# Kernel tuning notes

Hardware: AMD Instinct MI355X
Metric: run time of the kernel (lower is better)

Reference implementation:

```python
import jax, jax.numpy as jnp
import numpy as np


def _analytic_phase(x):
    """FFT-based analytic-signal phase, mean over channels. x: (B, C, T) -> (B, T)."""
    B, C, T = x.shape
    Xf = jnp.fft.fft(x, axis=-1)  # complex64
    # Hilbert multiplier: h[0]=1, h[1:T//2]=2, h[T//2]=1 (T even), rest 0
    h = np.zeros((T,), dtype=np.float32)
    h[0] = 1.0
    h[1:T // 2] = 2.0
    if T % 2 == 0:
        h[T // 2] = 1.0
    analytic = jnp.fft.ifft(Xf * jnp.asarray(h), axis=-1)
    phase = jnp.angle(analytic)          # (B, C, T)
    return phase.mean(axis=1)            # (B, T)


def setup_inputs() -> dict:
    key = jax.random.key(0)
    k = jax.random.split(key, 6)
    B, C, T = 32, 9, 4096
    num_codes, code_dim = 512, 64
    half = code_dim // 2
    s = 1.0 / np.sqrt(C)  # kaiming-uniform-ish scale for Linear(9, .)
    return {
        "imu_signal": jax.random.normal(k[0], (B, C, T), dtype=jnp.float32),
        "W_mag": jax.random.uniform(k[1], (half, C), jnp.float32, -s, s),
        "b_mag": jax.random.uniform(k[2], (half,), jnp.float32, -s, s),
        "W_phase": jax.random.uniform(k[3], (half, C), jnp.float32, -s, s),
        "b_phase": jax.random.uniform(k[4], (half,), jnp.float32, -s, s),
        "codebook": jax.random.normal(k[5], (num_codes, code_dim), dtype=jnp.float32),
    }


def reference(imu_signal, W_mag, b_mag, W_phase, b_phase, codebook):
    # imu_signal: (B, 9, T)
    phases = _analytic_phase(imu_signal)                      # (B, T)
    imu_btc = jnp.transpose(imu_signal, (0, 2, 1))            # (B, T, 9)

    mag_features = imu_btc @ W_mag.T + b_mag                  # (B, T, 32)

    phase_input = jnp.stack([jnp.cos(phases), jnp.sin(phases)], axis=-1)  # (B, T, 2)
    combined = jnp.concatenate([imu_btc[:, :, :7], phase_input], axis=-1)  # (B, T, 9)
    phase_features = combined @ W_phase.T + b_phase           # (B, T, 32)

    features = jnp.concatenate([mag_features, phase_features], axis=-1)  # (B, T, 64)

    # cdist argmin == argmin of squared distances: ||f||^2 - 2 f.c + ||c||^2
    d2 = (jnp.sum(features * features, axis=-1, keepdims=True)
          - 2.0 * jnp.einsum("btd,kd->btk", features, codebook)
          + jnp.sum(codebook * codebook, axis=-1))            # (B, T, K)
    indices = jnp.argmin(d2, axis=-1)                         # (B, T)
    quantized = codebook[indices]                             # (B, T, 64)
    return quantized, indices, phases
```

## Files before the change

### kernel.cpp

```cpp
#include <hip/hip_runtime.h>
#include <math.h>

#define TN 4096
#define HN 2048
#define NB 32
#define NCH 9
#define NCODES 512
#define CDIM 64
#define TAU 1e-3f
#define PTS 256
#define VQT 512

typedef _Float16 f16x8 __attribute__((ext_vector_type(8)));
typedef float f32x4 __attribute__((ext_vector_type(4)));

__device__ __forceinline__ float2 cmulf(float2 a, float2 b) {
    return make_float2(a.x * b.x - a.y * b.y, a.x * b.y + a.y * b.x);
}
__device__ __forceinline__ float2 f2add(float2 a, float2 b) {
    return make_float2(a.x + b.x, a.y + b.y);
}
__device__ __forceinline__ float2 f2sub(float2 a, float2 b) {
    return make_float2(a.x - b.x, a.y - b.y);
}

__device__ __forceinline__ unsigned long long packsi(float s, int i) {
    unsigned u = __float_as_uint(s);
    u = (u & 0x80000000u) ? ~u : (u | 0x80000000u);
    return ((unsigned long long)u << 32) | (unsigned)i;
}

__device__ __forceinline__ size_t aunit(int pbase, int plane, int s, int hi16, int l15) {
    return ((size_t)(((pbase * 2 + plane) * 2 + s) * 4 + hi16) << 4) + l15;
}

__global__ __launch_bounds__(256) void prep_kernel(const float* __restrict__ cb,
                                                   float* __restrict__ cn,
                                                   f16x8* __restrict__ ctiles,
                                                   float* __restrict__ ph) {
    const int bid = blockIdx.x;
    const int tid = threadIdx.x;
    if (bid < 512) {
        ph[bid * 256 + tid] = 0.0f;
        return;
    }
    if (bid < 544) {
        const int u = (bid - 512) * 256 + tid;
        const int l15 = u & 15;
        const int hi16 = (u >> 4) & 3;
        const int s = (u >> 6) & 1;
        const int plane = (u >> 7) & 1;
        const int cbase = u >> 8;
        const int code = cbase * 16 + l15;
        f16x8 out;
        #pragma unroll
        for (int e = 0; e < 8; ++e) {
            float c = cb[code * CDIM + 32 * s + 8 * hi16 + e];
            _Float16 hh = (_Float16)c;
            out[e] = plane ? (_Float16)(c - (float)hh) : hh;
        }
        ctiles[u] = out;
        return;
    }
    for (int k = tid; k < NCODES; k += 256) {
        const float4* c4 = (const float4*)(cb + (size_t)k * CDIM);
        float s = 0.0f;
        #pragma unroll
        for (int q = 0; q < 16; ++q) {
            float4 c = c4[q];
            s = fmaf(c.x, c.x, s);
            s = fmaf(c.y, c.y, s);
            s = fmaf(c.z, c.z, s);
            s = fmaf(c.w, c.w, s);
        }
        cn[k] = s;
    }
}

#define HT 512
__global__ __launch_bounds__(HT) void hilbert_phase_kernel(
    const float* __restrict__ x, float* __restrict__ phases) {
    __shared__ float2 bufA[TN];
    __shared__ float2 bufB[TN];
    __shared__ float2 tw[HN];
    const int tid = threadIdx.x;
    const int row1 = 2 * blockIdx.x;
    const int row2 = row1 + 1;
    const int b1 = row1 / NCH;
    const int b2 = row2 / NCH;
    const float* xr1 = x + (size_t)row1 * TN;
    const float* xr2 = x + (size_t)row2 * TN;

    for (int i = tid; i < HN; i += HT) {
        float ang = -3.14159265358979323846f * ((float)i / (float)HN);
        float s, c;
        sincosf(ang, &s, &c);
        tw[i] = make_float2(c, s);
    }
    for (int i = tid; i < TN; i += HT) {
        bufA[i] = make_float2(xr1[i], xr2[i]);
    }
    __syncthreads();

    float2* src = bufA;
    float2* dst = bufB;
    for (int stage = 0; stage < 6; ++stage) {
        const int m = 1 << (2 * stage);
        for (int idx = tid; idx < 1024; idx += HT) {
            const int kk = idx & (m - 1);
            const int jm = idx - kk;
            float2 a0 = src[idx];
            float2 a1 = src[idx + 1024];
            float2 a2 = src[idx + 2048];
            float2 a3 = src[idx + 3072];
            float2 b0 = f2add(a0, a2);
            float2 b1 = f2add(a1, a3);
            float2 b2 = f2sub(a0, a2);
            float2 b3 = f2sub(a1, a3);
            float2 w1 = tw[jm];
            float2 w2 = tw[2 * jm];
            float2 w3 = cmulf(w1, w2);
            float2 y0 = f2add(b0, b1);
            float2 mi = make_float2(b2.x + b3.y, b2.y - b3.x);
            float2 pi_ = make_float2(b2.x - b3.y, b2.y + b3.x);
            dst[4 * jm + kk]         = y0;
            dst[4 * jm + kk + m]     = cmulf(mi, w1);
            dst[4 * jm + kk + 2 * m] = cmulf(f2sub(b0, b1), w2);
            dst[4 * jm + kk + 3 * m] = cmulf(pi_, w3);
        }
        __syncthreads();
        float2* t0 = src; src = dst; dst = t0;
    }
    const float inv = 1.0f / (float)TN;
    for (int i = tid; i < TN; i += HT) {
        float sc;
        if (i == 0 || i == HN) sc = inv;
        else if (i < HN) sc = 2.0f * inv;
        else sc = 0.0f;
        float2 v = src[i];
        v.x *= sc; v.y *= sc;
        src[i] = v;
    }
    __syncthreads();
    for (int stage = 0; stage < 6; ++stage) {
        const int m = 1 << (2 * stage);
        for (int idx = tid; idx < 1024; idx += HT) {
            const int kk = idx & (m - 1);
            const int jm = idx - kk;
            float2 a0 = src[idx];
            float2 a1 = src[idx + 1024];
            float2 a2 = src[idx + 2048];
            float2 a3 = src[idx + 3072];
            float2 b0 = f2add(a0, a2);
            float2 b1 = f2add(a1, a3);
            float2 b2 = f2sub(a0, a2);
            float2 b3 = f2sub(a1, a3);
            float2 w1 = tw[jm];      w1.y = -w1.y;
            float2 w2 = tw[2 * jm];  w2.y = -w2.y;
            float2 w3 = cmulf(w1, w2);
            float2 y0 = f2add(b0, b1);
            float2 pi_ = make_float2(b2.x - b3.y, b2.y + b3.x);
            float2 mi = make_float2(b2.x + b3.y, b2.y - b3.x);
            dst[4 * jm + kk]         = y0;
            dst[4 * jm + kk + m]     = cmulf(pi_, w1);
            dst[4 * jm + kk + 2 * m] = cmulf(f2sub(b0, b1), w2);
            dst[4 * jm + kk + 3 * m] = cmulf(mi, w3);
        }
        __syncthreads();
        float2* t0 = src; src = dst; dst = t0;
    }
    float* ph1 = phases + (size_t)b1 * TN;
    float* ph2 = phases + (size_t)b2 * TN;
    for (int i = tid; i < TN; i += HT) {
        float2 d = src[i];
        float x1v = xr1[i];
        float x2v = xr2[i];
        atomicAdd(&ph1[i], atan2f(d.y - x2v, x1v) * (1.0f / 9.0f));
        atomicAdd(&ph2[i], atan2f(x1v - d.x, x2v) * (1.0f / 9.0f));
    }
}

__global__ __launch_bounds__(256) void feat_kernel(
    const float* __restrict__ imu,
    const float* __restrict__ Wm, const float* __restrict__ bm,
    const float* __restrict__ Wp, const float* __restrict__ bp,
    const float* __restrict__ phases,
    f16x8* __restrict__ atiles) {
    const int p = blockIdx.x * 256 + threadIdx.x;
    const int bb = p >> 12;
    const int tt = p & (TN - 1);
    float xc[9];
    #pragma unroll
    for (int c = 0; c < 9; ++c)
        xc[c] = imu[((size_t)(bb * 9 + c)) * TN + tt];
    float sp, cp;
    sincosf(phases[p], &sp, &cp);

    const int pbase = p >> 4;
    const int l15 = p & 15;
    #pragma unroll
    for (int g = 0; g < 8; ++g) {
        float v8[8];
        if (g < 4) {
            #pragma unroll
            for (int e = 0; e < 8; ++e) {
                const int j = 8 * g + e;
                float a = bm[j];
                #pragma unroll
                for (int c = 0; c < 9; ++c) a = fmaf(Wm[j * 9 + c], xc[c], a);
                v8[e] = a;
            }
        } else {
            #pragma unroll
            for (int e = 0; e < 8; ++e) {
                const int j = 8 * (g - 4) + e;
                float a = bp[j];
                #pragma unroll
                for (int c = 0; c < 7; ++c) a = fmaf(Wp[j * 9 + c], xc[c], a);
                a = fmaf(Wp[j * 9 + 7], cp, a);
                a = fmaf(Wp[j * 9 + 8], sp, a);
                v8[e] = a;
            }
        }
        f16x8 hv, lv;
        #pragma unroll
        for (int e = 0; e < 8; ++e) {
            _Float16 hh = (_Float16)v8[e];
            hv[e] = hh;
            lv[e] = (_Float16)(v8[e] - (float)hh);
        }
        const int s = g >> 2;
        const int hi16 = g & 3;
        atiles[aunit(pbase, 0, s, hi16, l15)] = hv;
        atiles[aunit(pbase, 1, s, hi16, l15)] = lv;
    }
}

#define MFMA16(A, B, C) __builtin_amdgcn_mfma_f32_16x16x32_f16((A), (B), (C), 0, 0, 0)

__global__ __launch_bounds__(VQT, 4) void vq_kernel(
    const float* __restrict__ imu,
    const float* __restrict__ Wm, const float* __restrict__ bm,
    const float* __restrict__ Wp, const float* __restrict__ bp,
    const float* __restrict__ cb,
    const float* __restrict__ cn,
    const f16x8* __restrict__ ctiles,
    const float* __restrict__ phases,
    const f16x8* atiles,
    float* out_q,
    float* __restrict__ out_i) {
    __shared__ float s_b[16][PTS];
    __shared__ float s_s[16][PTS];
    __shared__ int   s_i[16][PTS];
    __shared__ int s_idx[PTS];
    __shared__ float s_gap[PTS];
    const int tid = threadIdx.x;
    const int lane = tid & 63;
    const int w = tid >> 6;
    const int l15 = lane & 15;
    const int hi16 = lane >> 4;
    const int p0 = blockIdx.x * PTS;
    const int pb0 = p0 >> 4;

    for (int h = 0; h < 2; ++h) {
        const int kbase = 64 * w + 32 * h;
        const int cb0 = kbase >> 4;
        f16x8 cH00 = ctiles[aunit(cb0 + 0, 0, 0, hi16, l15)];
        f16x8 cH01 = ctiles[aunit(cb0 + 0, 0, 1, hi16, l15)];
        f16x8 cH10 = ctiles[aunit(cb0 + 1, 0, 0, hi16, l15)];
        f16x8 cH11 = ctiles[aunit(cb0 + 1, 0, 1, hi16, l15)];
        f16x8 cL00 = ctiles[aunit(cb0 + 0, 1, 0, hi16, l15)];
        f16x8 cL01 = ctiles[aunit(cb0 + 0, 1, 1, hi16, l15)];
        f16x8 cL10 = ctiles[aunit(cb0 + 1, 1, 0, hi16, l15)];
        f16x8 cL11 = ctiles[aunit(cb0 + 1, 1, 1, hi16, l15)];
        f32x4 cnv0 = *(const f32x4*)(cn + kbase + 4 * hi16);
        f32x4 cnv1 = *(const f32x4*)(cn + kbase + 16 + 4 * hi16);
        asm volatile("" : "+v"(cH00), "+v"(cH01), "+v"(cH10), "+v"(cH11),
                          "+v"(cL00), "+v"(cL01), "+v"(cL10), "+v"(cL11));
        asm volatile("" : "+v"(cnv0), "+v"(cnv1));

        #pragma unroll 2
        for (int cf = 0; cf < 16; ++cf) {
            const int pbase = pb0 + cf;
            f16x8 bH0 = atiles[aunit(pbase, 0, 0, hi16, l15)];
            f16x8 bH1 = atiles[aunit(pbase, 0, 1, hi16, l15)];
            f16x8 bL0 = atiles[aunit(pbase, 1, 0, hi16, l15)];
            f16x8 bL1 = atiles[aunit(pbase, 1, 1, hi16, l15)];
            f32x4 a0 = (f32x4){0.f, 0.f, 0.f, 0.f};
            f32x4 a1 = (f32x4){0.f, 0.f, 0.f, 0.f};
            a0 = MFMA16(cH00, bH0, a0);
            a0 = MFMA16(cH00, bL0, a0);
            a0 = MFMA16(cL00, bH0, a0);
            a0 = MFMA16(cH01, bH1, a0);
            a0 = MFMA16(cH01, bL1, a0);
            a0 = MFMA16(cL01, bH1, a0);
            a1 = MFMA16(cH10, bH0, a1);
            a1 = MFMA16(cH10, bL0, a1);
            a1 = MFMA16(cL10, bH0, a1);
            a1 = MFMA16(cH11, bH1, a1);
            a1 = MFMA16(cH11, bL1, a1);
            a1 = MFMA16(cL11, bH1, a1);
            float b = 3.4e38f, sec = 3.4e38f;
            int bi = 0;
            #pragma unroll
            for (int r = 0; r < 4; ++r) {
                float sc = fmaf(-2.0f, a0[r], cnv0[r]);
                const int ci = kbase + 4 * hi16 + r;
                bool lt = sc < b;
                sec = fminf(sec, lt ? b : sc);
                b = lt ? sc : b;
                bi = lt ? ci : bi;
            }
            #pragma unroll
            for (int r = 0; r < 4; ++r) {
                float sc = fmaf(-2.0f, a1[r], cnv1[r]);
                const int ci = kbase + 16 + 4 * hi16 + r;
                bool lt = sc < b;
                sec = fminf(sec, lt ? b : sc);
                b = lt ? sc : b;
                bi = lt ? ci : bi;
            }
            #pragma unroll
            for (int m = 16; m <= 32; m <<= 1) {
                float ob = __shfl_xor(b, m, 64);
                float os = __shfl_xor(sec, m, 64);
                int oi = __shfl_xor(bi, m, 64);
                float mx = fmaxf(b, ob);
                sec = fminf(fminf(sec, os), mx);
                bool take = (ob < b) || (ob == b && oi < bi);
                b = take ? ob : b;
                bi = take ? oi : bi;
            }
            if (hi16 == 0) {
                s_b[2 * w + h][16 * cf + l15] = b;
                s_s[2 * w + h][16 * cf + l15] = sec;
                s_i[2 * w + h][16 * cf + l15] = bi;
            }
        }
    }
    __syncthreads();

    if (tid < PTS) {
        float b = 3.4e38f, sec = 3.4e38f;
        int bi = 0;
        #pragma unroll 4
        for (int q = 0; q < 16; ++q) {
            float ob = s_b[q][tid];
            float os = s_s[q][tid];
            int oi = s_i[q][tid];
            float mx = fmaxf(b, ob);
            sec = fminf(fminf(sec, os), mx);
            bool take = (ob < b) || (ob == b && oi < bi);
            b = take ? ob : b;
            bi = take ? oi : bi;
        }
        s_idx[tid] = bi;
        out_i[p0 + tid] = (float)bi;
        s_gap[tid] = sec - b;
    }
    __syncthreads();

    {
        bool fl = (lane < 32) && (s_gap[32 * w + (lane & 31)] < TAU);
        unsigned long long bal = __ballot(fl);
        while (bal) {
            const int ln = __builtin_ctzll(bal);
            bal &= bal - 1;
            const int row = 32 * w + ln;
            const int pR = p0 + row;
            const int bbR = pR >> 12;
            const int ttR = pR & (TN - 1);
            float xcR[9];
            #pragma unroll
            for (int c = 0; c < 9; ++c)
                xcR[c] = imu[((size_t)(bbR * 9 + c)) * TN + ttR];
            float spR, cpR;
            sincosf(phases[pR], &spR, &cpR);
            float a0[8], a1[8], a2[8], a3[8];
            #pragma unroll
            for (int cc = 0; cc < 8; ++cc) {
                a0[cc] = 0.f; a1[cc] = 0.f; a2[cc] = 0.f; a3[cc] = 0.f;
            }
            for (int d4 = 0; d4 < 16; ++d4) {
                float fd[4];
                #pragma unroll
                for (int e = 0; e < 4; ++e) {
                    const int j = 4 * d4 + e;
                    float a;
                    if (j < 32) {
                        a = bm[j];
                        #pragma unroll
                        for (int c = 0; c < 9; ++c) a = fmaf(Wm[j * 9 + c], xcR[c], a);
                    } else {
                        const int jj = j - 32;
                        a = bp[jj];
                        #pragma unroll
                        for (int c = 0; c < 7; ++c) a = fmaf(Wp[jj * 9 + c], xcR[c], a);
                        a = fmaf(Wp[jj * 9 + 7], cpR, a);
                        a = fmaf(Wp[jj * 9 + 8], spR, a);
                    }
                    fd[e] = a;
                }
                #pragma unroll
                for (int cc = 0; cc < 8; ++cc) {
                    const float4 cv = ((const float4*)(cb + (size_t)(lane * 8 + cc) * CDIM))[d4];
                    a0[cc] = fmaf(fd[0], cv.x, a0[cc]);
                    a1[cc] = fmaf(fd[1], cv.y, a1[cc]);
                    a2[cc] = fmaf(fd[2], cv.z, a2[cc]);
                    a3[cc] = fmaf(fd[3], cv.w, a3[cc]);
                }
            }
            unsigned long long pbest = ~0ull;
            #pragma unroll
            for (int cc = 0; cc < 8; ++cc) {
                const int kk = lane * 8 + cc;
                float sc = fmaf(-2.0f, (a0[cc] + a1[cc]) + (a2[cc] + a3[cc]), cn[kk]);
                unsigned long long pk = packsi(sc, kk);
                pbest = pk < pbest ? pk : pbest;
            }
            #pragma unroll
            for (int m = 1; m <= 32; m <<= 1) {
                unsigned long long o = __shfl_xor(pbest, m, 64);
                pbest = o < pbest ? o : pbest;
            }
            if (lane == 0) {
                const int bi = (int)(pbest & 0xFFFFFFFFu);
                s_idx[row] = bi;
                out_i[p0 + row] = (float)bi;
            }
        }
    }
    __syncthreads();

    float4* oq = (float4*)out_q;
    const float4* c4g = (const float4*)cb;
    for (int i = tid; i < PTS * 16; i += VQT) {
        const int pt = i >> 4;
        const int q = i & 15;
        oq[(size_t)(p0 + pt) * 16 + q] = c4g[(size_t)s_idx[pt] * 16 + q];
    }
}

extern "C" void kernel_launch(void* const* d_in, const int* in_sizes, int n_in,
                              void* d_out, int out_size, void* d_ws, size_t ws_size,
                              hipStream_t stream) {
    const float* imu = (const float*)d_in[0];
    const float* Wm  = (const float*)d_in[1];
    const float* bm  = (const float*)d_in[2];
    const float* Wp  = (const float*)d_in[3];
    const float* bp  = (const float*)d_in[4];
    const float* cb  = (const float*)d_in[5];

    float* out_q = (float*)d_out;
    float* out_i = out_q + (size_t)NB * TN * CDIM;
    float* out_p = out_i + (size_t)NB * TN;

    float* cn     = (float*)d_ws;
    f16x8* ctiles = (f16x8*)((char*)d_ws + 2048);
    f16x8* atiles = (f16x8*)out_q;

    prep_kernel<<<545, 256, 0, stream>>>(cb, cn, ctiles, out_p);
    hilbert_phase_kernel<<<NB * NCH / 2, HT, 0, stream>>>(imu, out_p);
    feat_kernel<<<(NB * TN) / 256, 256, 0, stream>>>(imu, Wm, bm, Wp, bp, out_p, atiles);
    vq_kernel<<<(NB * TN) / PTS, VQT, 0, stream>>>(imu, Wm, bm, Wp, bp, cb,
                                                   cn, ctiles, out_p, atiles,
                                                   out_q, out_i);
}
```

Measured before the change: 171.9 us.

## Stage point tiles in LDS and widen per-wave code tile to 64 codes

The VQ kernel now copies the block's 256-point split-f16 feature tiles into shared memory with async global-to-LDS loads, instead of each wave re-reading them from global memory twice. Each wave keeps 64 codes' hi/lo fragments in registers and computes four 16x16 accumulators per point group in one pass. This halves the partial-argmin slots to merge. More resident registers and 64KB of LDS drop the occupancy hint from 4 to 2 blocks per CU, trading occupancy for less redundant memory traffic.

```diff
diff --git a/kernel.cpp b/kernel.cpp
--- a/kernel.cpp
+++ b/kernel.cpp
@@ -28,6 +28,12 @@
     unsigned u = __float_as_uint(s);
     u = (u & 0x80000000u) ? ~u : (u | 0x80000000u);
     return ((unsigned long long)u << 32) | (unsigned)i;
+}
+
+__device__ __forceinline__ void gload_lds16(const void* g, void* l) {
+    __builtin_amdgcn_global_load_lds(
+        (const __attribute__((address_space(1))) unsigned int*)g,
+        (__attribute__((address_space(3))) unsigned int*)l, 16, 0, 0);
 }
 
 __device__ __forceinline__ size_t aunit(int pbase, int plane, int s, int hi16, int l15) {
@@ -238,7 +244,7 @@
 
 #define MFMA16(A, B, C) __builtin_amdgcn_mfma_f32_16x16x32_f16((A), (B), (C), 0, 0, 0)
 
-__global__ __launch_bounds__(VQT, 4) void vq_kernel(
+__global__ __launch_bounds__(VQT, 2) void vq_kernel(
     const float* __restrict__ imu,
     const float* __restrict__ Wm, const float* __restrict__ bm,
     const float* __restrict__ Wp, const float* __restrict__ bp,
@@ -249,9 +255,10 @@
     const f16x8* atiles,
     float* out_q,
     float* __restrict__ out_i) {
-    __shared__ float s_b[16][PTS];
-    __shared__ float s_s[16][PTS];
-    __shared__ int   s_i[16][PTS];
+    __shared__ __align__(16) f16x8 sPT[16 * 256];
+    __shared__ float s_b[8][PTS];
+    __shared__ float s_s[8][PTS];
+    __shared__ int   s_i[8][PTS];
     __shared__ int s_idx[PTS];
     __shared__ float s_gap[PTS];
     const int tid = threadIdx.x;
@@ -262,80 +269,78 @@
     const int p0 = blockIdx.x * PTS;
     const int pb0 = p0 >> 4;
 
-    for (int h = 0; h < 2; ++h) {
-        const int kbase = 64 * w + 32 * h;
-        const int cb0 = kbase >> 4;
-        f16x8 cH00 = ctiles[aunit(cb0 + 0, 0, 0, hi16, l15)];
-        f16x8 cH01 = ctiles[aunit(cb0 + 0, 0, 1, hi16, l15)];
-        f16x8 cH10 = ctiles[aunit(cb0 + 1, 0, 0, hi16, l15)];
-        f16x8 cH11 = ctiles[aunit(cb0 + 1, 0, 1, hi16, l15)];
-        f16x8 cL00 = ctiles[aunit(cb0 + 0, 1, 0, hi16, l15)];
-        f16x8 cL01 = ctiles[aunit(cb0 + 0, 1, 1, hi16, l15)];
-        f16x8 cL10 = ctiles[aunit(cb0 + 1, 1, 0, hi16, l15)];
-        f16x8 cL11 = ctiles[aunit(cb0 + 1, 1, 1, hi16, l15)];
-        f32x4 cnv0 = *(const f32x4*)(cn + kbase + 4 * hi16);
-        f32x4 cnv1 = *(const f32x4*)(cn + kbase + 16 + 4 * hi16);
-        asm volatile("" : "+v"(cH00), "+v"(cH01), "+v"(cH10), "+v"(cH11),
-                          "+v"(cL00), "+v"(cL01), "+v"(cL10), "+v"(cL11));
-        asm volatile("" : "+v"(cnv0), "+v"(cnv1));
-
-        #pragma unroll 2
-        for (int cf = 0; cf < 16; ++cf) {
-            const int pbase = pb0 + cf;
-            f16x8 bH0 = atiles[aunit(pbase, 0, 0, hi16, l15)];
-            f16x8 bH1 = atiles[aunit(pbase, 0, 1, hi16, l15)];
-            f16x8 bL0 = atiles[aunit(pbase, 1, 0, hi16, l15)];
-            f16x8 bL1 = atiles[aunit(pbase, 1, 1, hi16, l15)];
-            f32x4 a0 = (f32x4){0.f, 0.f, 0.f, 0.f};
-            f32x4 a1 = (f32x4){0.f, 0.f, 0.f, 0.f};
-            a0 = MFMA16(cH00, bH0, a0);
-            a0 = MFMA16(cH00, bL0, a0);
-            a0 = MFMA16(cL00, bH0, a0);
-            a0 = MFMA16(cH01, bH1, a0);
-            a0 = MFMA16(cH01, bL1, a0);
-            a0 = MFMA16(cL01, bH1, a0);
-            a1 = MFMA16(cH10, bH0, a1);
-            a1 = MFMA16(cH10, bL0, a1);
-            a1 = MFMA16(cL10, bH0, a1);
-            a1 = MFMA16(cH11, bH1, a1);
-            a1 = MFMA16(cH11, bL1, a1);
-            a1 = MFMA16(cL11, bH1, a1);
-            float b = 3.4e38f, sec = 3.4e38f;
-            int bi = 0;
+    {
+        const char* gsrc = (const char*)(atiles + (size_t)pb0 * 256);
+        char* ldst = (char*)sPT;
+        #pragma unroll
+        for (int i = 0; i < 8; ++i) {
+            const int u = i * VQT + tid;
+            gload_lds16(gsrc + (size_t)u * 16, ldst + u * 16);
+        }
+    }
+
+    const int kbase = 64 * w;
+    f16x8 cH[4][2], cL[4][2];
+    #pragma unroll
+    for (int rf = 0; rf < 4; ++rf) {
+        #pragma unroll
+        for (int s = 0; s < 2; ++s) {
+            cH[rf][s] = ctiles[aunit(4 * w + rf, 0, s, hi16, l15)];
+            cL[rf][s] = ctiles[aunit(4 * w + rf, 1, s, hi16, l15)];
+        }
+    }
+    f32x4 cnv[4];
+    #pragma unroll
+    for (int rf = 0; rf < 4; ++rf)
+        cnv[rf] = *(const f32x4*)(cn + kbase + 16 * rf + 4 * hi16);
+    __syncthreads();
+
+    for (int cf = 0; cf < 16; ++cf) {
+        f16x8 bH0 = sPT[cf * 256 + 0 * 128 + 0 * 64 + lane];
+        f16x8 bH1 = sPT[cf * 256 + 0 * 128 + 1 * 64 + lane];
+        f16x8 bL0 = sPT[cf * 256 + 1 * 128 + 0 * 64 + lane];
+        f16x8 bL1 = sPT[cf * 256 + 1 * 128 + 1 * 64 + lane];
+        f32x4 acc[4];
+        #pragma unroll
+        for (int rf = 0; rf < 4; ++rf) acc[rf] = (f32x4){0.f, 0.f, 0.f, 0.f};
+        #pragma unroll
+        for (int rf = 0; rf < 4; ++rf) {
+            acc[rf] = MFMA16(cH[rf][0], bH0, acc[rf]);
+            acc[rf] = MFMA16(cH[rf][0], bL0, acc[rf]);
+            acc[rf] = MFMA16(cL[rf][0], bH0, acc[rf]);
+            acc[rf] = MFMA16(cH[rf][1], bH1, acc[rf]);
+            acc[rf] = MFMA16(cH[rf][1], bL1, acc[rf]);
+            acc[rf] = MFMA16(cL[rf][1], bH1, acc[rf]);
+        }
+        float b = 3.4e38f, sec = 3.4e38f;
+        int bi = 0;
+        #pragma unroll
+        for (int rf = 0; rf < 4; ++rf) {
             #pragma unroll
             for (int r = 0; r < 4; ++r) {
-                float sc = fmaf(-2.0f, a0[r], cnv0[r]);
-                const int ci = kbase + 4 * hi16 + r;
+                float sc = fmaf(-2.0f, acc[rf][r], cnv[rf][r]);
+                const int ci = kbase + 16 * rf + 4 * hi16 + r;
                 bool lt = sc < b;
                 sec = fminf(sec, lt ? b : sc);
                 b = lt ? sc : b;
                 bi = lt ? ci : bi;
             }
-            #pragma unroll
-            for (int r = 0; r < 4; ++r) {
-                float sc = fmaf(-2.0f, a1[r], cnv1[r]);
-                const int ci = kbase + 16 + 4 * hi16 + r;
-                bool lt = sc < b;
-                sec = fminf(sec, lt ? b : sc);
-                b = lt ? sc : b;
-                bi = lt ? ci : bi;
-            }
-            #pragma unroll
-            for (int m = 16; m <= 32; m <<= 1) {
-                float ob = __shfl_xor(b, m, 64);
-                float os = __shfl_xor(sec, m, 64);
-                int oi = __shfl_xor(bi, m, 64);
-                float mx = fmaxf(b, ob);
-                sec = fminf(fminf(sec, os), mx);
-                bool take = (ob < b) || (ob == b && oi < bi);
-                b = take ? ob : b;
-                bi = take ? oi : bi;
-            }
-            if (hi16 == 0) {
-                s_b[2 * w + h][16 * cf + l15] = b;
-                s_s[2 * w + h][16 * cf + l15] = sec;
-                s_i[2 * w + h][16 * cf + l15] = bi;
-            }
+        }
+        #pragma unroll
+        for (int m = 16; m <= 32; m <<= 1) {
+            float ob = __shfl_xor(b, m, 64);
+            float os = __shfl_xor(sec, m, 64);
+            int oi = __shfl_xor(bi, m, 64);
+            float mx = fmaxf(b, ob);
+            sec = fminf(fminf(sec, os), mx);
+            bool take = (ob < b) || (ob == b && oi < bi);
+            b = take ? ob : b;
+            bi = take ? oi : bi;
+        }
+        if (hi16 == 0) {
+            s_b[w][16 * cf + l15] = b;
+            s_s[w][16 * cf + l15] = sec;
+            s_i[w][16 * cf + l15] = bi;
         }
     }
     __syncthreads();
@@ -344,7 +349,7 @@
         float b = 3.4e38f, sec = 3.4e38f;
         int bi = 0;
         #pragma unroll 4
-        for (int q = 0; q < 16; ++q) {
+        for (int q = 0; q < 8; ++q) {
             float ob = s_b[q][tid];
             float os = s_s[q][tid];
             int oi = s_i[q][tid];
```

Result: slower. 178.6 us (+3.9%).
